# Kernel tuning notes

Hardware: AMD Instinct MI355X
Metric: run time of the kernel (lower is better)

The kernel has to match this reference:

```python
import jax, jax.numpy as jnp
import numpy as np

EMBED_DIM = 1024
NUM_HEADS = 16
HEAD_DIM = EMBED_DIM // NUM_HEADS
SPARSITY_LAMBDA = 0.01
B, S = 2, 2048


def setup_inputs() -> dict:
    key = jax.random.key(0)
    ks = jax.random.split(key, 10)
    scale = 0.02
    inp = {
        "x": jax.random.normal(ks[0], (B, S, EMBED_DIM), dtype=jnp.float32),
        "Wq": jax.random.normal(ks[1], (EMBED_DIM, EMBED_DIM), dtype=jnp.float32) * scale,
        "bq": jnp.zeros((EMBED_DIM,), dtype=jnp.float32),
        "Wk": jax.random.normal(ks[2], (EMBED_DIM, EMBED_DIM), dtype=jnp.float32) * scale,
        "bk": jnp.zeros((EMBED_DIM,), dtype=jnp.float32),
        "Wv": jax.random.normal(ks[3], (EMBED_DIM, EMBED_DIM), dtype=jnp.float32) * scale,
        "bv": jnp.zeros((EMBED_DIM,), dtype=jnp.float32),
        "Wo": jax.random.normal(ks[4], (EMBED_DIM, EMBED_DIM), dtype=jnp.float32) * scale,
        "bo": jnp.zeros((EMBED_DIM,), dtype=jnp.float32),
        "z": jax.random.normal(ks[5], (NUM_HEADS,), dtype=jnp.float32),
    }
    return inp


def reference(x, Wq, bq, Wk, bk, Wv, bv, Wo, bo, z):
    # Linear layers (torch Linear: y = x @ W.T + b); W here stored as [out, in]
    def split_heads(t):  # [B,S,E] -> [B,H,S,D]
        return t.reshape(B, S, NUM_HEADS, HEAD_DIM).transpose(0, 2, 1, 3)

    q = split_heads(x @ Wq.T + bq)
    k = split_heads(x @ Wk.T + bk)
    v = split_heads(x @ Wv.T + bv)

    scores = jnp.einsum("bhsd,bhtd->bhst", q, k) / jnp.sqrt(jnp.float32(HEAD_DIM))
    gate = jax.nn.sigmoid(z)  # [H], per-head scalar gate on raw scores
    scores = scores * gate[None, :, None, None]
    probs = jax.nn.softmax(scores, axis=-1)
    ctx = jnp.einsum("bhst,bhtd->bhsd", probs, v)  # [B,H,S,D]
    ctx = ctx.transpose(0, 2, 1, 3).reshape(B, S, EMBED_DIM)
    out = ctx @ Wo.T + bo
    penalty = jnp.sum(jax.nn.sigmoid(z)) * SPARSITY_LAMBDA
    return out, penalty
```

## Files before the change

### kernel.cpp

```cpp
#include <hip/hip_runtime.h>

typedef unsigned short ushort_t;
typedef __bf16 bf16x8 __attribute__((ext_vector_type(8)));
typedef ushort_t u16x8 __attribute__((ext_vector_type(8)));
typedef float f32x4 __attribute__((ext_vector_type(4)));
typedef unsigned int u32x2 __attribute__((ext_vector_type(2)));

#define DEVI __device__ __forceinline__

constexpr int Ed = 1024;
constexpr int Hh = 16;
constexpr int Dd = 64;
constexpr int Ss = 2048;
constexpr int Mm = 4096;

constexpr int NX4 = Mm * Ed / 4;
constexpr int NW4 = Ed * Ed / 4;

DEVI ushort_t f2bf(float f) {
    union { float f; unsigned int i; } v; v.f = f;
    unsigned int r = v.i + 0x7fffu + ((v.i >> 16) & 1u);
    return (ushort_t)(r >> 16);
}
DEVI ushort_t f2bf_hi(float f) {
    union { float f; unsigned int i; } v; v.f = f;
    return (ushort_t)(v.i >> 16);
}
DEVI unsigned int fbits(float f) {
    union { float f; unsigned int i; } v; v.f = f;
    return v.i;
}
DEVI float fast_exp2(float x) {
    float r;
    asm("v_exp_f32 %0, %1" : "=v"(r) : "v"(x));
    return r;
}

__global__ __launch_bounds__(256) void cvt_all(
    const float* __restrict__ x,  const float* __restrict__ Wq,
    const float* __restrict__ Wk, const float* __restrict__ Wv,
    const float* __restrict__ Wo,
    ushort_t* __restrict__ xb,  ushort_t* __restrict__ Wqb,
    ushort_t* __restrict__ Wkb, ushort_t* __restrict__ Wvb,
    ushort_t* __restrict__ Wob)
{
    int i = blockIdx.x * 256 + threadIdx.x;
    const float* s; ushort_t* d; int off;
    if (i < NX4)                { s = x;  d = xb;  off = i; }
    else if (i < NX4 + NW4)     { s = Wq; d = Wqb; off = i - NX4; }
    else if (i < NX4 + 2 * NW4) { s = Wk; d = Wkb; off = i - NX4 - NW4; }
    else if (i < NX4 + 3 * NW4) { s = Wv; d = Wvb; off = i - NX4 - 2 * NW4; }
    else                        { s = Wo; d = Wob; off = i - NX4 - 3 * NW4; }
    float4 v = ((const float4*)s)[off];
    ushort4 o; o.x = f2bf(v.x); o.y = f2bf(v.y); o.z = f2bf(v.z); o.w = f2bf(v.w);
    ((ushort4*)d)[off] = o;
}

DEVI void gld16(const void* g, void* l) {
    __builtin_amdgcn_global_load_lds(
        (__attribute__((address_space(1))) void*)(g),
        (__attribute__((address_space(3))) void*)(l), 16, 0, 0);
}

DEVI void gemm_core(const ushort_t* __restrict__ A, const ushort_t* __restrict__ W,
                    ushort_t* As, ushort_t* Bs, int tm, int tn, int K,
                    f32x4 acc[4][4])
{
    const int tid  = threadIdx.x;
    const int w    = tid >> 6;
    const int lane = tid & 63;
    const int quad = lane >> 4;
    const int l15  = lane & 15;
    const int wy   = w >> 1, wx = w & 1;
    const int rowc = lane >> 3;
    const int col8s = (((lane & 7) ^ rowc) * 8);
    const int swq  = l15 & 7;

    for (int k0 = 0; k0 < K; k0 += 64) {
        __syncthreads();
#pragma unroll
        for (int i = 0; i < 4; ++i) {
            int chunk = w * 4 + i;
            int row = chunk * 8 + rowc;
            gld16(A + (size_t)(tm + row) * K + k0 + col8s, (char*)As + chunk * 1024);
            gld16(W + (size_t)(tn + row) * K + k0 + col8s, (char*)Bs + chunk * 1024);
        }
        __syncthreads();
#pragma unroll
        for (int ks = 0; ks < 64; ks += 32) {
            const int k4 = ks >> 3;
            bf16x8 a[4], b[4];
#pragma unroll
            for (int mi = 0; mi < 4; ++mi)
                a[mi] = *(const bf16x8*)&As[(wy * 64 + mi * 16 + l15) * 64
                                            + (((quad + k4) ^ swq) * 8)];
#pragma unroll
            for (int ni = 0; ni < 4; ++ni)
                b[ni] = *(const bf16x8*)&Bs[(wx * 64 + ni * 16 + l15) * 64
                                            + (((quad + k4) ^ swq) * 8)];
#pragma unroll
            for (int mi = 0; mi < 4; ++mi)
#pragma unroll
                for (int ni = 0; ni < 4; ++ni)
                    acc[mi][ni] = __builtin_amdgcn_mfma_f32_16x16x32_bf16(
                        a[mi], b[ni], acc[mi][ni], 0, 0, 0);
        }
    }
}

__global__ __launch_bounds__(256, 3) void qkv_gemm(
    const ushort_t* __restrict__ x,
    const ushort_t* __restrict__ Wq, const float* __restrict__ bq,
    const ushort_t* __restrict__ Wk, const float* __restrict__ bk,
    const ushort_t* __restrict__ Wv, const float* __restrict__ bv,
    ushort_t* __restrict__ qo, ushort_t* __restrict__ ko, ushort_t* __restrict__ vto)
{
    __shared__ __align__(16) ushort_t As[128 * 64];
    __shared__ __align__(16) ushort_t Bs[128 * 64];
    const ushort_t* W; const float* bias; ushort_t* outp; int vmode;
    if (blockIdx.z == 0)      { W = Wq; bias = bq; outp = qo;  vmode = 0; }
    else if (blockIdx.z == 1) { W = Wk; bias = bk; outp = ko;  vmode = 0; }
    else                      { W = Wv; bias = bv; outp = vto; vmode = 1; }

    const int tm = blockIdx.x * 128, tn = blockIdx.y * 128;
    f32x4 acc[4][4] = {};
    gemm_core(x, W, As, Bs, tm, tn, Ed, acc);

    const int tid = threadIdx.x, w = tid >> 6, lane = tid & 63;
    const int quad = lane >> 4, l15 = lane & 15;
    const int wy = w >> 1, wx = w & 1;
    if (vmode == 0) {
#pragma unroll
        for (int ni = 0; ni < 4; ++ni) {
            int gc = tn + wx * 64 + ni * 16 + l15;
            float bb = bias[gc];
            int h = gc >> 6, d = gc & 63;
#pragma unroll
            for (int mi = 0; mi < 4; ++mi) {
#pragma unroll
                for (int r = 0; r < 4; ++r) {
                    int gr = tm + wy * 64 + mi * 16 + quad * 4 + r;
                    int b_ = gr >> 11, s_ = gr & 2047;
                    float v = acc[mi][ni][r] + bb;
                    outp[((size_t)(b_ * Hh + h) * Ss + s_) * Dd + d] = f2bf_hi(v);
                }
            }
        }
    } else {
#pragma unroll
        for (int ni = 0; ni < 4; ++ni) {
            int gc = tn + wx * 64 + ni * 16 + l15;
            float bb = bias[gc];
            int h = gc >> 6, d = gc & 63;
#pragma unroll
            for (int mi = 0; mi < 4; ++mi) {
                int gr0 = tm + wy * 64 + mi * 16 + quad * 4;
                int b_ = gr0 >> 11, s0 = gr0 & 2047;
                unsigned int u0 = fbits(acc[mi][ni][0] + bb);
                unsigned int u1 = fbits(acc[mi][ni][1] + bb);
                unsigned int u2 = fbits(acc[mi][ni][2] + bb);
                unsigned int u3 = fbits(acc[mi][ni][3] + bb);
                u32x2 pk;
                pk[0] = (u1 & 0xffff0000u) | (u0 >> 16);
                pk[1] = (u3 & 0xffff0000u) | (u2 >> 16);
                *(u32x2*)&outp[((size_t)(b_ * Hh + h) * Dd + d) * Ss + s0] = pk;
            }
        }
    }
}

__global__ __launch_bounds__(256, 3) void out_gemm(
    const ushort_t* __restrict__ ctx, const ushort_t* __restrict__ Wo,
    const float* __restrict__ bo, const float* __restrict__ z,
    float* __restrict__ out)
{
    __shared__ __align__(16) ushort_t As[128 * 64];
    __shared__ __align__(16) ushort_t Bs[64 * 64];
    const int tm = blockIdx.x * 128, tn = blockIdx.y * 64;

    const int tid  = threadIdx.x;
    const int w    = tid >> 6;
    const int lane = tid & 63;
    const int quad = lane >> 4;
    const int l15  = lane & 15;
    const int wy   = w >> 1, wx = w & 1;
    const int rowc = lane >> 3;
    const int col8s = (((lane & 7) ^ rowc) * 8);
    const int swq  = l15 & 7;

    f32x4 acc[4][2] = {};
    for (int k0 = 0; k0 < Ed; k0 += 64) {
        __syncthreads();
#pragma unroll
        for (int i = 0; i < 4; ++i) {
            int chunk = w * 4 + i;
            int row = chunk * 8 + rowc;
            gld16(ctx + (size_t)(tm + row) * Ed + k0 + col8s, (char*)As + chunk * 1024);
        }
#pragma unroll
        for (int i = 0; i < 2; ++i) {
            int chunk = w * 2 + i;
            int row = chunk * 8 + rowc;
            gld16(Wo + (size_t)(tn + row) * Ed + k0 + col8s, (char*)Bs + chunk * 1024);
        }
        __syncthreads();
#pragma unroll
        for (int ks = 0; ks < 64; ks += 32) {
            const int k4 = ks >> 3;
            bf16x8 a[4], b[2];
#pragma unroll
            for (int mi = 0; mi < 4; ++mi)
                a[mi] = *(const bf16x8*)&As[(wy * 64 + mi * 16 + l15) * 64
                                            + (((quad + k4) ^ swq) * 8)];
#pragma unroll
            for (int ni = 0; ni < 2; ++ni)
                b[ni] = *(const bf16x8*)&Bs[(wx * 32 + ni * 16 + l15) * 64
                                            + (((quad + k4) ^ swq) * 8)];
#pragma unroll
            for (int mi = 0; mi < 4; ++mi)
#pragma unroll
                for (int ni = 0; ni < 2; ++ni)
                    acc[mi][ni] = __builtin_amdgcn_mfma_f32_16x16x32_bf16(
                        a[mi], b[ni], acc[mi][ni], 0, 0, 0);
        }
    }

#pragma unroll
    for (int ni = 0; ni < 2; ++ni) {
        int gc = tn + wx * 32 + ni * 16 + l15;
        float bb = bo[gc];
#pragma unroll
        for (int mi = 0; mi < 4; ++mi)
#pragma unroll
            for (int r = 0; r < 4; ++r) {
                int gr = tm + wy * 64 + mi * 16 + quad * 4 + r;
                out[(size_t)gr * Ed + gc] = acc[mi][ni][r] + bb;
            }
    }

    if (blockIdx.x == 0 && blockIdx.y == 0 && tid == 0) {
        float s = 0.f;
        for (int hh = 0; hh < Hh; ++hh) s += 1.f / (1.f + __expf(-z[hh]));
        out[(size_t)Mm * Ed] = s * 0.01f;
    }
}

__global__ __launch_bounds__(256, 2) void attn(
    const ushort_t* __restrict__ Q, const ushort_t* __restrict__ Kk,
    const ushort_t* __restrict__ Vt, const float* __restrict__ z,
    ushort_t* __restrict__ ctx)
{
    __shared__ __align__(16) ushort_t Ks[2][128 * 64];
    __shared__ __align__(16) ushort_t Ps[4][32 * 68];

    const int tid = threadIdx.x, w = tid >> 6, lane = tid & 63;
    const int quad = lane >> 4, l15 = lane & 15;
    const int lin = blockIdx.x + 16 * blockIdx.y;
    const int qt = lin >> 5;
    const int bh = (lin & 7) * 4 + ((lin >> 3) & 3);
    const int h = bh & (Hh - 1), b_ = bh >> 4;
    const size_t base = (size_t)bh * Ss * Dd;

    const float gate = 1.f / (1.f + __expf(-z[h]));
    const float scl2 = gate * 0.125f * 1.44269504f;

    bf16x8 aQ[2][2];
#pragma unroll
    for (int m = 0; m < 2; ++m)
#pragma unroll
        for (int c = 0; c < 2; ++c)
            aQ[m][c] = *(const bf16x8*)&Q[base
                + (size_t)(qt * 128 + w * 32 + m * 16 + l15) * Dd + c * 32 + quad * 8];

    const int rowc = lane >> 3;
    const int gs   = ((lane & 7) ^ rowc) * 8;
    const ushort_t* kSrc[4];
#pragma unroll
    for (int i = 0; i < 4; ++i)
        kSrc[i] = Kk + base + (size_t)(w * 32 + i * 8 + rowc) * Dd + gs;
    const ushort_t* vBase = Vt + base + (size_t)l15 * Ss + quad * 8;

    f32x4 accO[2][4] = {};
    float lsum[2][4] = {};

    const int swq = (l15 & 7) * 8;

#pragma unroll
    for (int i = 0; i < 4; ++i)
        gld16(kSrc[i], (char*)Ks[0] + (w * 4 + i) * 1024);

    for (int kt = 0; kt < Ss / 128; ++kt) {
        const int cur = kt & 1, nxt = cur ^ 1;
        __syncthreads();

        if (kt + 1 < Ss / 128) {
#pragma unroll
            for (int i = 0; i < 4; ++i)
                gld16(kSrc[i] + (size_t)(kt + 1) * 128 * Dd,
                      (char*)Ks[nxt] + (w * 4 + i) * 1024);
        }

#pragma unroll
        for (int sub = 0; sub < 2; ++sub) {
            bf16x8 vf[2][4];
#pragma unroll
            for (int ni = 0; ni < 4; ++ni) {
                const ushort_t* vp = vBase + (size_t)(ni * 16) * Ss + kt * 128 + sub * 64;
                vf[0][ni] = *(const bf16x8*)(vp);
                vf[1][ni] = *(const bf16x8*)(vp + 32);
            }

            f32x4 sAcc[2][4] = {};
            __builtin_amdgcn_s_setprio(1);
#pragma unroll
            for (int ni = 0; ni < 4; ++ni) {
                bf16x8 b0 = *(const bf16x8*)&Ks[cur][(sub * 64 + ni * 16 + l15) * 64 + ((quad * 8) ^ swq)];
                bf16x8 b1 = *(const bf16x8*)&Ks[cur][(sub * 64 + ni * 16 + l15) * 64 + (((quad + 4) * 8) ^ swq)];
#pragma unroll
                for (int m = 0; m < 2; ++m) {
                    sAcc[m][ni] = __builtin_amdgcn_mfma_f32_16x16x32_bf16(aQ[m][0], b0, sAcc[m][ni], 0, 0, 0);
                    sAcc[m][ni] = __builtin_amdgcn_mfma_f32_16x16x32_bf16(aQ[m][1], b1, sAcc[m][ni], 0, 0, 0);
                }
            }
            __builtin_amdgcn_s_setprio(0);

#pragma unroll
            for (int m = 0; m < 2; ++m)
#pragma unroll
                for (int ni = 0; ni < 4; ++ni)
#pragma unroll
                    for (int r = 0; r < 4; ++r) {
                        float p = fast_exp2(sAcc[m][ni][r] * scl2);
                        lsum[m][r] += p;
                        Ps[w][(m * 16 + quad * 4 + r) * 68 + ni * 16 + l15] = f2bf_hi(p);
                    }

            __builtin_amdgcn_s_setprio(1);
#pragma unroll
            for (int c = 0; c < 2; ++c) {
                bf16x8 aP0 = *(const bf16x8*)&Ps[w][l15 * 68 + c * 32 + quad * 8];
                bf16x8 aP1 = *(const bf16x8*)&Ps[w][(16 + l15) * 68 + c * 32 + quad * 8];
#pragma unroll
                for (int ni = 0; ni < 4; ++ni) {
                    accO[0][ni] = __builtin_amdgcn_mfma_f32_16x16x32_bf16(aP0, vf[c][ni], accO[0][ni], 0, 0, 0);
                    accO[1][ni] = __builtin_amdgcn_mfma_f32_16x16x32_bf16(aP1, vf[c][ni], accO[1][ni], 0, 0, 0);
                }
            }
            __builtin_amdgcn_s_setprio(0);
        }
    }

#pragma unroll
    for (int m = 0; m < 2; ++m)
#pragma unroll
        for (int r = 0; r < 4; ++r) {
            lsum[m][r] += __shfl_xor(lsum[m][r], 1);
            lsum[m][r] += __shfl_xor(lsum[m][r], 2);
            lsum[m][r] += __shfl_xor(lsum[m][r], 4);
            lsum[m][r] += __shfl_xor(lsum[m][r], 8);
        }

#pragma unroll
    for (int m = 0; m < 2; ++m)
#pragma unroll
        for (int r = 0; r < 4; ++r) {
            int srow = qt * 128 + w * 32 + m * 16 + quad * 4 + r;
            float inv = 1.f / lsum[m][r];
#pragma unroll
            for (int ni = 0; ni < 4; ++ni) {
                int d = ni * 16 + l15;
                ctx[((size_t)(b_ * Ss + srow)) * Ed + h * Dd + d] = f2bf_hi(accO[m][ni][r] * inv);
            }
        }
}

extern "C" void kernel_launch(void* const* d_in, const int* in_sizes, int n_in,
                              void* d_out, int out_size, void* d_ws, size_t ws_size,
                              hipStream_t stream) {
    const float* x  = (const float*)d_in[0];
    const float* Wq = (const float*)d_in[1];
    const float* bq = (const float*)d_in[2];
    const float* Wk = (const float*)d_in[3];
    const float* bk = (const float*)d_in[4];
    const float* Wv = (const float*)d_in[5];
    const float* bv = (const float*)d_in[6];
    const float* Wo = (const float*)d_in[7];
    const float* bo = (const float*)d_in[8];
    const float* z  = (const float*)d_in[9];
    float* out = (float*)d_out;

    ushort_t* xb  = (ushort_t*)d_ws;
    ushort_t* Wqb = xb  + (size_t)Mm * Ed;
    ushort_t* Wkb = Wqb + (size_t)Ed * Ed;
    ushort_t* Wvb = Wkb + (size_t)Ed * Ed;
    ushort_t* Wob = Wvb + (size_t)Ed * Ed;
    ushort_t* qw  = Wob + (size_t)Ed * Ed;
    ushort_t* kw  = qw + (size_t)Mm * Ed;
    ushort_t* vT  = kw + (size_t)Mm * Ed;
    ushort_t* cx  = vT + (size_t)Mm * Ed;

    dim3 blk(256);
    cvt_all<<<dim3((NX4 + 4 * NW4) / 256), blk, 0, stream>>>(
        x, Wq, Wk, Wv, Wo, xb, Wqb, Wkb, Wvb, Wob);
    qkv_gemm<<<dim3(Mm / 128, Ed / 128, 3), blk, 0, stream>>>(
        xb, Wqb, bq, Wkb, bk, Wvb, bv, qw, kw, vT);
    attn<<<dim3(Ss / 128, 2 * Hh), blk, 0, stream>>>(qw, kw, vT, z, cx);
    out_gemm<<<dim3(Mm / 128, Ed / 64), blk, 0, stream>>>(cx, Wob, bo, z, out);
}
```

Before: 209.6 us.

## Split attention key tiles across two wave groups and fold gate scale into Q

```diff
diff --git a/kernel.cpp b/kernel.cpp
--- a/kernel.cpp
+++ b/kernel.cpp
@@ -34,6 +34,9 @@
     float r;
     asm("v_exp_f32 %0, %1" : "=v"(r) : "v"(x));
     return r;
+}
+DEVI unsigned int pkbf(float lo, float hi) {
+    return (fbits(hi) & 0xffff0000u) | (fbits(lo) >> 16);
 }
 
 __global__ __launch_bounds__(256) void cvt_all(
@@ -113,6 +116,7 @@
     const ushort_t* __restrict__ Wq, const float* __restrict__ bq,
     const ushort_t* __restrict__ Wk, const float* __restrict__ bk,
     const ushort_t* __restrict__ Wv, const float* __restrict__ bv,
+    const float* __restrict__ z,
     ushort_t* __restrict__ qo, ushort_t* __restrict__ ko, ushort_t* __restrict__ vto)
 {
     __shared__ __align__(16) ushort_t As[128 * 64];
@@ -135,13 +139,16 @@
             int gc = tn + wx * 64 + ni * 16 + l15;
             float bb = bias[gc];
             int h = gc >> 6, d = gc & 63;
+            float sc = 1.f;
+            if (blockIdx.z == 0)
+                sc = (1.f / (1.f + __expf(-z[h]))) * 0.18033688f;
 #pragma unroll
             for (int mi = 0; mi < 4; ++mi) {
 #pragma unroll
                 for (int r = 0; r < 4; ++r) {
                     int gr = tm + wy * 64 + mi * 16 + quad * 4 + r;
                     int b_ = gr >> 11, s_ = gr & 2047;
-                    float v = acc[mi][ni][r] + bb;
+                    float v = (acc[mi][ni][r] + bb) * sc;
                     outp[((size_t)(b_ * Hh + h) * Ss + s_) * Dd + d] = f2bf_hi(v);
                 }
             }
@@ -156,13 +163,9 @@
             for (int mi = 0; mi < 4; ++mi) {
                 int gr0 = tm + wy * 64 + mi * 16 + quad * 4;
                 int b_ = gr0 >> 11, s0 = gr0 & 2047;
-                unsigned int u0 = fbits(acc[mi][ni][0] + bb);
-                unsigned int u1 = fbits(acc[mi][ni][1] + bb);
-                unsigned int u2 = fbits(acc[mi][ni][2] + bb);
-                unsigned int u3 = fbits(acc[mi][ni][3] + bb);
                 u32x2 pk;
-                pk[0] = (u1 & 0xffff0000u) | (u0 >> 16);
-                pk[1] = (u3 & 0xffff0000u) | (u2 >> 16);
+                pk[0] = pkbf(acc[mi][ni][0] + bb, acc[mi][ni][1] + bb);
+                pk[1] = pkbf(acc[mi][ni][2] + bb, acc[mi][ni][3] + bb);
                 *(u32x2*)&outp[((size_t)(b_ * Hh + h) * Dd + d) * Ss + s0] = pk;
             }
         }
@@ -245,39 +248,38 @@
     }
 }
 
-__global__ __launch_bounds__(256, 2) void attn(
+__global__ __launch_bounds__(512, 4) void attn(
     const ushort_t* __restrict__ Q, const ushort_t* __restrict__ Kk,
     const ushort_t* __restrict__ Vt, const float* __restrict__ z,
     ushort_t* __restrict__ ctx)
 {
-    __shared__ __align__(16) ushort_t Ks[2][128 * 64];
-    __shared__ __align__(16) ushort_t Ps[4][32 * 68];
+    __shared__ __align__(16) char SM[67584];
+    ushort_t* KsBuf = (ushort_t*)SM;
 
     const int tid = threadIdx.x, w = tid >> 6, lane = tid & 63;
+    const int wg = w >> 2;
+    const int wi = w & 3;
     const int quad = lane >> 4, l15 = lane & 15;
+    ushort_t* Ps_w = (ushort_t*)(SM + 32768) + w * (32 * 68);
+
     const int lin = blockIdx.x + 16 * blockIdx.y;
     const int qt = lin >> 5;
     const int bh = (lin & 7) * 4 + ((lin >> 3) & 3);
     const int h = bh & (Hh - 1), b_ = bh >> 4;
     const size_t base = (size_t)bh * Ss * Dd;
 
-    const float gate = 1.f / (1.f + __expf(-z[h]));
-    const float scl2 = gate * 0.125f * 1.44269504f;
-
     bf16x8 aQ[2][2];
 #pragma unroll
     for (int m = 0; m < 2; ++m)
 #pragma unroll
         for (int c = 0; c < 2; ++c)
             aQ[m][c] = *(const bf16x8*)&Q[base
-                + (size_t)(qt * 128 + w * 32 + m * 16 + l15) * Dd + c * 32 + quad * 8];
+                + (size_t)(qt * 128 + wi * 32 + m * 16 + l15) * Dd + c * 32 + quad * 8];
 
     const int rowc = lane >> 3;
     const int gs   = ((lane & 7) ^ rowc) * 8;
-    const ushort_t* kSrc[4];
-#pragma unroll
-    for (int i = 0; i < 4; ++i)
-        kSrc[i] = Kk + base + (size_t)(w * 32 + i * 8 + rowc) * Dd + gs;
+    const ushort_t* kSrcA = Kk + base + (size_t)((w * 2 + 0) * 8 + rowc) * Dd + gs;
+    const ushort_t* kSrcB = Kk + base + (size_t)((w * 2 + 1) * 8 + rowc) * Dd + gs;
     const ushort_t* vBase = Vt + base + (size_t)l15 * Ss + quad * 8;
 
     f32x4 accO[2][4] = {};
@@ -285,93 +287,118 @@
 
     const int swq = (l15 & 7) * 8;
 
-#pragma unroll
-    for (int i = 0; i < 4; ++i)
-        gld16(kSrc[i], (char*)Ks[0] + (w * 4 + i) * 1024);
+    gld16(kSrcA, (char*)KsBuf + (w * 2 + 0) * 1024);
+    gld16(kSrcB, (char*)KsBuf + (w * 2 + 1) * 1024);
 
     for (int kt = 0; kt < Ss / 128; ++kt) {
         const int cur = kt & 1, nxt = cur ^ 1;
         __syncthreads();
 
         if (kt + 1 < Ss / 128) {
-#pragma unroll
-            for (int i = 0; i < 4; ++i)
-                gld16(kSrc[i] + (size_t)(kt + 1) * 128 * Dd,
-                      (char*)Ks[nxt] + (w * 4 + i) * 1024);
-        }
-
-#pragma unroll
-        for (int sub = 0; sub < 2; ++sub) {
-            bf16x8 vf[2][4];
+            gld16(kSrcA + (size_t)(kt + 1) * 128 * Dd,
+                  (char*)KsBuf + (nxt * 128 * 64 + (w * 2 + 0) * 512) * 2);
+            gld16(kSrcB + (size_t)(kt + 1) * 128 * Dd,
+                  (char*)KsBuf + (nxt * 128 * 64 + (w * 2 + 1) * 512) * 2);
+        }
+
+        const ushort_t* KsC = KsBuf + cur * 128 * 64;
+
+        f32x4 sAcc[2][4] = {};
+        __builtin_amdgcn_s_setprio(1);
+#pragma unroll
+        for (int ni = 0; ni < 4; ++ni) {
+            bf16x8 b0 = *(const bf16x8*)&KsC[(wg * 64 + ni * 16 + l15) * 64 + ((quad * 8) ^ swq)];
+            bf16x8 b1 = *(const bf16x8*)&KsC[(wg * 64 + ni * 16 + l15) * 64 + (((quad + 4) * 8) ^ swq)];
+#pragma unroll
+            for (int m = 0; m < 2; ++m) {
+                sAcc[m][ni] = __builtin_amdgcn_mfma_f32_16x16x32_bf16(aQ[m][0], b0, sAcc[m][ni], 0, 0, 0);
+                sAcc[m][ni] = __builtin_amdgcn_mfma_f32_16x16x32_bf16(aQ[m][1], b1, sAcc[m][ni], 0, 0, 0);
+            }
+        }
+        __builtin_amdgcn_s_setprio(0);
+
+#pragma unroll
+        for (int m = 0; m < 2; ++m)
+#pragma unroll
+            for (int ni = 0; ni < 4; ++ni)
+#pragma unroll
+                for (int r = 0; r < 4; ++r) {
+                    float p = fast_exp2(sAcc[m][ni][r]);
+                    lsum[m][r] += p;
+                    Ps_w[(m * 16 + quad * 4 + r) * 68 + ni * 16 + l15] = f2bf_hi(p);
+                }
+
+        bf16x8 vf[2][4];
+#pragma unroll
+        for (int ni = 0; ni < 4; ++ni) {
+            const ushort_t* vp = vBase + (size_t)(ni * 16) * Ss + kt * 128 + wg * 64;
+            vf[0][ni] = *(const bf16x8*)(vp);
+            vf[1][ni] = *(const bf16x8*)(vp + 32);
+        }
+
+        __builtin_amdgcn_s_setprio(1);
+#pragma unroll
+        for (int c = 0; c < 2; ++c) {
+            bf16x8 aP0 = *(const bf16x8*)&Ps_w[l15 * 68 + c * 32 + quad * 8];
+            bf16x8 aP1 = *(const bf16x8*)&Ps_w[(16 + l15) * 68 + c * 32 + quad * 8];
 #pragma unroll
             for (int ni = 0; ni < 4; ++ni) {
-                const ushort_t* vp = vBase + (size_t)(ni * 16) * Ss + kt * 128 + sub * 64;
-                vf[0][ni] = *(const bf16x8*)(vp);
-                vf[1][ni] = *(const bf16x8*)(vp + 32);
-            }
-
-            f32x4 sAcc[2][4] = {};
-            __builtin_amdgcn_s_setprio(1);
-#pragma unroll
-            for (int ni = 0; ni < 4; ++ni) {
-                bf16x8 b0 = *(const bf16x8*)&Ks[cur][(sub * 64 + ni * 16 + l15) * 64 + ((quad * 8) ^ swq)];
-                bf16x8 b1 = *(const bf16x8*)&Ks[cur][(sub * 64 + ni * 16 + l15) * 64 + (((quad + 4) * 8) ^ swq)];
-#pragma unroll
-                for (int m = 0; m < 2; ++m) {
-                    sAcc[m][ni] = __builtin_amdgcn_mfma_f32_16x16x32_bf16(aQ[m][0], b0, sAcc[m][ni], 0, 0, 0);
-                    sAcc[m][ni] = __builtin_amdgcn_mfma_f32_16x16x32_bf16(aQ[m][1], b1, sAcc[m][ni], 0, 0, 0);
+                accO[0][ni] = __builtin_amdgcn_mfma_f32_16x16x32_bf16(aP0, vf[c][ni], accO[0][ni], 0, 0, 0);
+                accO[1][ni] = __builtin_amdgcn_mfma_f32_16x16x32_bf16(aP1, vf[c][ni], accO[1][ni], 0, 0, 0);
+            }
+        }
+        __builtin_amdgcn_s_setprio(0);
+    }
+
+    __syncthreads();
+    float* ex = (float*)SM;
+    const int slot = (wi * 64 + lane) * 41;
+    if (wg == 1) {
+#pragma unroll
+        for (int m = 0; m < 2; ++m)
+#pragma unroll
+            for (int ni = 0; ni < 4; ++ni)
+#pragma unroll
+                for (int r = 0; r < 4; ++r)
+                    ex[slot + m * 16 + ni * 4 + r] = accO[m][ni][r];
+#pragma unroll
+        for (int m = 0; m < 2; ++m)
+#pragma unroll
+            for (int r = 0; r < 4; ++r)
+                ex[slot + 32 + m * 4 + r] = lsum[m][r];
+    }
+    __syncthreads();
+    if (wg == 0) {
+#pragma unroll
+        for (int m = 0; m < 2; ++m)
+#pragma unroll
+            for (int ni = 0; ni < 4; ++ni)
+#pragma unroll
+                for (int r = 0; r < 4; ++r)
+                    accO[m][ni][r] += ex[slot + m * 16 + ni * 4 + r];
+#pragma unroll
+        for (int m = 0; m < 2; ++m)
+#pragma unroll
+            for (int r = 0; r < 4; ++r) {
+                lsum[m][r] += ex[slot + 32 + m * 4 + r];
+                lsum[m][r] += __shfl_xor(lsum[m][r], 1);
+                lsum[m][r] += __shfl_xor(lsum[m][r], 2);
+                lsum[m][r] += __shfl_xor(lsum[m][r], 4);
+                lsum[m][r] += __shfl_xor(lsum[m][r], 8);
+            }
+#pragma unroll
+        for (int m = 0; m < 2; ++m)
+#pragma unroll
+            for (int r = 0; r < 4; ++r) {
+                int srow = qt * 128 + wi * 32 + m * 16 + quad * 4 + r;
+                float inv = 1.f / lsum[m][r];
+#pragma unroll
+                for (int ni = 0; ni < 4; ++ni) {
+                    int d = ni * 16 + l15;
+                    ctx[((size_t)(b_ * Ss + srow)) * Ed + h * Dd + d] = f2bf_hi(accO[m][ni][r] * inv);
                 }
             }
-            __builtin_amdgcn_s_setprio(0);
-
-#pragma unroll
-            for (int m = 0; m < 2; ++m)
-#pragma unroll
-                for (int ni = 0; ni < 4; ++ni)
-#pragma unroll
-                    for (int r = 0; r < 4; ++r) {
-                        float p = fast_exp2(sAcc[m][ni][r] * scl2);
-                        lsum[m][r] += p;
-                        Ps[w][(m * 16 + quad * 4 + r) * 68 + ni * 16 + l15] = f2bf_hi(p);
-                    }
-
-            __builtin_amdgcn_s_setprio(1);
-#pragma unroll
-            for (int c = 0; c < 2; ++c) {
-                bf16x8 aP0 = *(const bf16x8*)&Ps[w][l15 * 68 + c * 32 + quad * 8];
-                bf16x8 aP1 = *(const bf16x8*)&Ps[w][(16 + l15) * 68 + c * 32 + quad * 8];
-#pragma unroll
-                for (int ni = 0; ni < 4; ++ni) {
-                    accO[0][ni] = __builtin_amdgcn_mfma_f32_16x16x32_bf16(aP0, vf[c][ni], accO[0][ni], 0, 0, 0);
-                    accO[1][ni] = __builtin_amdgcn_mfma_f32_16x16x32_bf16(aP1, vf[c][ni], accO[1][ni], 0, 0, 0);
-                }
-            }
-            __builtin_amdgcn_s_setprio(0);
-        }
-    }
-
-#pragma unroll
-    for (int m = 0; m < 2; ++m)
-#pragma unroll
-        for (int r = 0; r < 4; ++r) {
-            lsum[m][r] += __shfl_xor(lsum[m][r], 1);
-            lsum[m][r] += __shfl_xor(lsum[m][r], 2);
-            lsum[m][r] += __shfl_xor(lsum[m][r], 4);
-            lsum[m][r] += __shfl_xor(lsum[m][r], 8);
-        }
-
-#pragma unroll
-    for (int m = 0; m < 2; ++m)
-#pragma unroll
-        for (int r = 0; r < 4; ++r) {
-            int srow = qt * 128 + w * 32 + m * 16 + quad * 4 + r;
-            float inv = 1.f / lsum[m][r];
-#pragma unroll
-            for (int ni = 0; ni < 4; ++ni) {
-                int d = ni * 16 + l15;
-                ctx[((size_t)(b_ * Ss + srow)) * Ed + h * Dd + d] = f2bf_hi(accO[m][ni][r] * inv);
-            }
-        }
+    }
 }
 
 extern "C" void kernel_launch(void* const* d_in, const int* in_sizes, int n_in,
@@ -399,11 +426,10 @@
     ushort_t* vT  = kw + (size_t)Mm * Ed;
     ushort_t* cx  = vT + (size_t)Mm * Ed;
 
-    dim3 blk(256);
-    cvt_all<<<dim3((NX4 + 4 * NW4) / 256), blk, 0, stream>>>(
+    cvt_all<<<dim3((NX4 + 4 * NW4) / 256), dim3(256), 0, stream>>>(
         x, Wq, Wk, Wv, Wo, xb, Wqb, Wkb, Wvb, Wob);
-    qkv_gemm<<<dim3(Mm / 128, Ed / 128, 3), blk, 0, stream>>>(
-        xb, Wqb, bq, Wkb, bk, Wvb, bv, qw, kw, vT);
-    attn<<<dim3(Ss / 128, 2 * Hh), blk, 0, stream>>>(qw, kw, vT, z, cx);
-    out_gemm<<<dim3(Mm / 128, Ed / 64), blk, 0, stream>>>(cx, Wob, bo, z, out);
-}
+    qkv_gemm<<<dim3(Mm / 128, Ed / 128, 3), dim3(256), 0, stream>>>(
+        xb, Wqb, bq, Wkb, bk, Wvb, bv, z, qw, kw, vT);
+    attn<<<dim3(Ss / 128, 2 * Hh), dim3(512), 0, stream>>>(qw, kw, vT, z, cx);
+    out_gemm<<<dim3(Mm / 128, Ed / 64), dim3(256), 0, stream>>>(cx, Wob, bo, z, out);
+}
```

Measured after the change: 211.7 us. Within noise of the previous version (+1.0%).
